# Kernel optimization log

Hardware: AMD Instinct MI355X
Metric: run time of the kernel (lower is better)

## Reference

```python
import jax, jax.numpy as jnp
import numpy as np

DIM = 768
HEADS = 8
HEAD_DIM = DIM // HEADS
SCALE = HEAD_DIM ** -0.5
EPS = 1e-5


def layernorm(x, gamma, beta):
    mu = jnp.mean(x, axis=-1, keepdims=True)
    var = jnp.mean((x - mu) ** 2, axis=-1, keepdims=True)
    return (x - mu) * jax.lax.rsqrt(var + EPS) * gamma + beta


def setup_inputs() -> dict:
    key = jax.random.key(0)
    ks = jax.random.split(key, 12)
    B, L, M, D = 8, 1024, 1024, DIM
    s = D ** -0.5
    return {
        "x": jax.random.normal(ks[0], (B, L, D), jnp.float32),
        "context": jax.random.normal(ks[1], (B, M, D), jnp.float32),
        "Wq": jax.random.normal(ks[2], (D, D), jnp.float32) * s,
        "bq": jnp.zeros((D,), jnp.float32),
        "Wkv": jax.random.normal(ks[3], (D, 2 * D), jnp.float32) * s,
        "bkv": jnp.zeros((2 * D,), jnp.float32),
        "Wp": jax.random.normal(ks[4], (D, D), jnp.float32) * s,
        "bp": jnp.zeros((D,), jnp.float32),
        "g1": jnp.ones((D,), jnp.float32),
        "b1": jnp.zeros((D,), jnp.float32),
        "g2": jnp.ones((D,), jnp.float32),
        "b2": jnp.zeros((D,), jnp.float32),
    }


def reference(x, context, Wq, bq, Wkv, bkv, Wp, bp, g1, b1, g2, b2):
    B, L, D = x.shape
    M = context.shape[1]
    Hp = Wp_ = int(L ** 0.5)
    x_n = layernorm(x, g1, b1)
    c_n = layernorm(context, g2, b2)
    q = (x_n @ Wq + bq).reshape(B, L, HEADS, HEAD_DIM).transpose(0, 2, 1, 3)  # bhld
    kv = (c_n @ Wkv + bkv).reshape(B, M, 2, HEADS, HEAD_DIM).transpose(2, 0, 3, 1, 4)
    k, v = kv[0], kv[1]  # bhmd
    attn = jnp.einsum("bhld,bhmd->bhlm", q, k) * SCALE
    w = jax.nn.softmax(attn, axis=-1)
    attn_map = w.mean(axis=1).sum(axis=-1).reshape(B, Hp, Wp_)
    out = jnp.einsum("bhlm,bhmd->bhld", w, v).transpose(0, 2, 1, 3).reshape(B, L, D)
    out = out @ Wp + bp
    # dropout is identity in eval mode (training=False)
    return out + x, attn_map
```

## Files before the change

kernel.cpp:

```cpp
#include <hip/hip_runtime.h>

typedef unsigned short u16;
typedef short bf16x8 __attribute__((ext_vector_type(8)));
typedef float f32x4 __attribute__((ext_vector_type(4)));
typedef unsigned short u16x8 __attribute__((ext_vector_type(8)));
typedef unsigned short u16x4 __attribute__((ext_vector_type(4)));

union bfr { unsigned int u[4]; bf16x8 v; };

__device__ __forceinline__ u16 f2bf(float f) {
    unsigned int u = __builtin_bit_cast(unsigned int, f);
    u = (u + 0x7fffu + ((u >> 16) & 1u)) >> 16;
    return (u16)u;
}

__device__ __forceinline__ unsigned int cvtpk(float lo, float hi) {
    unsigned int r;
    asm("v_cvt_pk_bf16_f32 %0, %1, %2" : "=v"(r) : "v"(lo), "v"(hi));
    return r;
}

__device__ __forceinline__ void gload16(const u16* src, u16* lds_dst) {
    __builtin_amdgcn_global_load_lds(
        (const __attribute__((address_space(1))) unsigned int*)src,
        (__attribute__((address_space(3))) unsigned int*)lds_dst, 16, 0, 0);
}

__global__ __launch_bounds__(256) void prep_ln_k(
    const float* __restrict__ x, const float* __restrict__ ctx,
    const float* __restrict__ g1, const float* __restrict__ b1,
    const float* __restrict__ g2, const float* __restrict__ b2,
    const float* __restrict__ Wq, const float* __restrict__ Wkv,
    const float* __restrict__ Wp,
    u16* __restrict__ xn, u16* __restrict__ cn,
    u16* __restrict__ WqT, u16* __restrict__ WkvT, u16* __restrict__ WpT)
{
    const int id = blockIdx.x;
    const int t = threadIdx.x;
    if (id >= 16384) {
        __shared__ float T[64][65];
        int t2 = id - 16384;
        const float* src; u16* dst; int lds, k0, n0;
        if (t2 < 288) { src = Wkv; dst = WkvT; lds = 1536; k0 = (t2 / 24) * 64; n0 = (t2 % 24) * 64; }
        else if (t2 < 432) { int u = t2 - 288; src = Wq; dst = WqT; lds = 768; k0 = (u / 12) * 64; n0 = (u % 12) * 64; }
        else { int u = t2 - 432; src = Wp; dst = WpT; lds = 768; k0 = (u / 12) * 64; n0 = (u % 12) * 64; }
        const int rr = t >> 4, c4 = (t & 15) * 4;
        #pragma unroll
        for (int it = 0; it < 4; it++) {
            int r = rr + it * 16;
            f32x4 v = *(const f32x4*)&src[(long)(k0 + r) * lds + n0 + c4];
            #pragma unroll
            for (int j = 0; j < 4; j++) T[c4 + j][r] = v[j];
        }
        __syncthreads();
        #pragma unroll
        for (int it = 0; it < 4; it++) {
            int r = rr + it * 16;
            u16x4 w;
            #pragma unroll
            for (int j = 0; j < 4; j++) w[j] = f2bf(T[r][c4 + j]);
            *(u16x4*)&dst[(long)(n0 + r) * 768 + k0 + c4] = w;
        }
        return;
    }
    const float* src; const float* g; const float* b; u16* dst;
    if (id < 8192) { src = x + (long)id * 768; g = g1; b = b1; dst = xn + (long)id * 768; }
    else { int r = id - 8192; src = ctx + (long)r * 768; g = g2; b = b2; dst = cn + (long)r * 768; }

    int lane = t & 63, wid = t >> 6;
    float v0 = src[t], v1 = src[t + 256], v2 = src[t + 512];
    float s = v0 + v1 + v2;
    for (int o = 32; o; o >>= 1) s += __shfl_xor(s, o);
    __shared__ float r1[4], r2[4];
    if (!lane) r1[wid] = s;
    __syncthreads();
    float mu = (r1[0] + r1[1] + r1[2] + r1[3]) * (1.0f / 768.0f);
    float d0 = v0 - mu, d1 = v1 - mu, d2 = v2 - mu;
    float q = d0 * d0 + d1 * d1 + d2 * d2;
    for (int o = 32; o; o >>= 1) q += __shfl_xor(q, o);
    if (!lane) r2[wid] = q;
    __syncthreads();
    float var = (r2[0] + r2[1] + r2[2] + r2[3]) * (1.0f / 768.0f);
    float rs = rsqrtf(var + 1e-5f);
    dst[t]       = f2bf(d0 * rs * g[t]       + b[t]);
    dst[t + 256] = f2bf(d1 * rs * g[t + 256] + b[t + 256]);
    dst[t + 512] = f2bf(d2 * rs * g[t + 512] + b[t + 512]);
}

__global__ __launch_bounds__(256) void qkv_k(
    const u16* __restrict__ xn, const u16* __restrict__ cn,
    const u16* __restrict__ WqT, const u16* __restrict__ WkvT,
    const float* __restrict__ bq, const float* __restrict__ bkv,
    u16* __restrict__ Qb, u16* __restrict__ Kb, u16* __restrict__ Vt)
{
    __shared__ u16 As[128 * 32];
    __shared__ u16 Bs[128 * 32];
    const int id = blockIdx.x;
    const int swz = (id & 7) * 144 + (id >> 3);
    const int tid = threadIdx.x, lane = tid & 63, wid = tid >> 6;
    const int wr = wid >> 1, wc = wid & 1;
    const int g = lane >> 4, i15 = lane & 15;

    const bool isQ = swz < 384;
    int rt, ct;
    const u16* A; const u16* Bt; const float* bias;
    if (isQ) { rt = swz / 6;  ct = swz % 6;  A = xn; Bt = WqT;  bias = bq; }
    else { int s2 = swz - 384; rt = s2 / 12; ct = s2 % 12; A = cn; Bt = WkvT; bias = bkv; }
    const int row0 = rt * 128, col0 = ct * 128;

    const u16* srcA[2]; const u16* srcB[2]; int ldsOff[2];
    #pragma unroll
    for (int c = 0; c < 2; c++) {
        int P0 = (wid * 2 + c) * 1024;
        int P = P0 + lane * 16;
        int r = P >> 6, colx = (P & 63) >> 1;
        srcA[c] = A  + (long)(row0 + r) * 768 + colx;
        srcB[c] = Bt + (long)(col0 + r) * 768 + colx;
        ldsOff[c] = P0 >> 1;
    }

    f32x4 acc[4][4] = {};
    for (int k0 = 0; k0 < 768; k0 += 32) {
        __syncthreads();
        #pragma unroll
        for (int c = 0; c < 2; c++) {
            gload16(srcA[c] + k0, &As[ldsOff[c]]);
            gload16(srcB[c] + k0, &Bs[ldsOff[c]]);
        }
        __syncthreads();
        bf16x8 av[4], bv[4];
        #pragma unroll
        for (int m = 0; m < 4; m++)
            av[m] = *(const bf16x8*)&As[(wr * 64 + m * 16 + i15) * 32 + g * 8];
        #pragma unroll
        for (int n = 0; n < 4; n++)
            bv[n] = *(const bf16x8*)&Bs[(wc * 64 + n * 16 + i15) * 32 + g * 8];
        #pragma unroll
        for (int m = 0; m < 4; m++)
            #pragma unroll
            for (int n = 0; n < 4; n++)
                acc[m][n] = __builtin_amdgcn_mfma_f32_16x16x32_bf16(av[m], bv[n], acc[m][n], 0, 0, 0);
    }

    float bv4[4];
    #pragma unroll
    for (int n = 0; n < 4; n++) bv4[n] = bias[col0 + wc * 64 + n * 16 + i15];

    #pragma unroll
    for (int m = 0; m < 4; m++) {
        #pragma unroll
        for (int n = 0; n < 4; n++) {
            const int col = col0 + wc * 64 + n * 16 + i15;
            #pragma unroll
            for (int r = 0; r < 4; r++) {
                const int row = row0 + wr * 64 + m * 16 + g * 4 + r;
                float v = acc[m][n][r];
                if (isQ) {
                    v = (v + bv4[n]) * 0.14724444706f;
                    int b = row >> 10, l = row & 1023;
                    int h = col / 96, d = col % 96;
                    Qb[((long)(b * 8 + h) * 1024 + l) * 96 + d] = f2bf(v);
                } else {
                    v += bv4[n];
                    int b = row >> 10, mt = row & 1023;
                    if (col < 768) {
                        int h = col / 96, d = col % 96;
                        Kb[((long)(b * 8 + h) * 1024 + mt) * 96 + d] = f2bf(v);
                    } else {
                        int cc = col - 768;
                        int h = cc / 96, d = cc % 96;
                        Vt[((long)(b * 8 + h) * 96 + d) * 1024 + mt] = f2bf(v);
                    }
                }
            }
        }
    }
}

__global__ __launch_bounds__(256) void flash_k(
    const u16* __restrict__ Qb, const u16* __restrict__ Kb,
    const u16* __restrict__ Vt, u16* __restrict__ Ob)
{
    const int i = blockIdx.x;
    const int s8 = i >> 3;
    const int bh = (i & 7) * 8 + (s8 >> 4);
    const int qt = s8 & 15;
    const int tid = threadIdx.x, lane = tid & 63, wid = tid >> 6;
    const int g = lane >> 4, i15 = lane & 15;

    __shared__ u16 Ks[2][6144];
    __shared__ u16 Vs[2][6144];

    const long baseQK = (long)bh * 98304;
    const u16* Kt  = Kb + baseQK;
    const u16* Vtp = Vt + baseQK;

    bf16x8 qf[3];
    {
        const u16* qrow = Qb + baseQK + (long)(qt * 64 + wid * 16 + i15) * 96 + g * 8;
        qf[0] = *(const bf16x8*)(qrow);
        qf[1] = *(const bf16x8*)(qrow + 32);
        qf[2] = *(const bf16x8*)(qrow + 64);
    }

    int krd[4];
    #pragma unroll
    for (int n = 0; n < 4; n++) {
        int q4 = i15 >> 2, rr = i15 & 3, m = n >> 1;
        int R = (n & 1) ? (m * 32 + ((q4 ^ 2) << 3) + 4 + rr)
                        : (m * 32 + (q4 << 3) + rr);
        krd[n] = R * 32 + g * 8;
    }
    int vrd[6][2];
    #pragma unroll
    for (int n6 = 0; n6 < 6; n6++) {
        int row = n6 * 16 + i15;
        #pragma unroll
        for (int kk = 0; kk < 2; kk++)
            vrd[n6][kk] = row * 64 + ((kk * 32 + g * 8) ^ ((row & 7) << 3));
    }

    int kgo[3], kwr[3], vgo[3], vwr[3];
    #pragma unroll
    for (int it = 0; it < 3; it++) {
        int e = tid + it * 256;
        int r = e / 12, cEl = (e % 12) * 8;
        kgo[it] = r * 96 + cEl;
        kwr[it] = (cEl >> 5) * 2048 + r * 32 + (cEl & 31);
        int d = e >> 3, m8 = (e & 7) * 8;
        vgo[it] = d * 1024 + m8;
        vwr[it] = d * 64 + (m8 ^ ((d & 7) << 3));
    }

    u16x8 kreg[3], vreg[3];
    #pragma unroll
    for (int it = 0; it < 3; it++) {
        kreg[it] = *(const u16x8*)&Kt[kgo[it]];
        vreg[it] = *(const u16x8*)&Vtp[vgo[it]];
    }
    #pragma unroll
    for (int it = 0; it < 3; it++) {
        *(u16x8*)&Ks[0][kwr[it]] = kreg[it];
        *(u16x8*)&Vs[0][vwr[it]] = vreg[it];
    }

    f32x4 o[6] = {};
    float lsum = 0.f;
    int cur = 0;

    for (int t = 0; t < 16; t++) {
        __syncthreads();
        if (t < 15) {
            #pragma unroll
            for (int it = 0; it < 3; it++) {
                kreg[it] = *(const u16x8*)&Kt[(t + 1) * 6144 + kgo[it]];
                vreg[it] = *(const u16x8*)&Vtp[(t + 1) * 64 + vgo[it]];
            }
        }

        f32x4 s[4] = {};
        #pragma unroll
        for (int kd = 0; kd < 3; kd++) {
            #pragma unroll
            for (int n = 0; n < 4; n++) {
                bf16x8 kf = *(const bf16x8*)&Ks[cur][kd * 2048 + krd[n]];
                s[n] = __builtin_amdgcn_mfma_f32_16x16x32_bf16(kf, qf[kd], s[n], 0, 0, 0);
            }
        }

        unsigned int pk[4][2];
        #pragma unroll
        for (int n = 0; n < 4; n++) {
            float p0 = exp2f(s[n][0]), p1 = exp2f(s[n][1]);
            float p2 = exp2f(s[n][2]), p3 = exp2f(s[n][3]);
            lsum += (p0 + p1) + (p2 + p3);
            pk[n][0] = cvtpk(p0, p1);
            pk[n][1] = cvtpk(p2, p3);
        }

        #pragma unroll
        for (int kk = 0; kk < 2; kk++) {
            bfr pa;
            pa.u[0] = pk[kk * 2][0];
            pa.u[1] = pk[kk * 2][1];
            pa.u[2] = __shfl_xor(pk[kk * 2 + 1][0], 32);
            pa.u[3] = __shfl_xor(pk[kk * 2 + 1][1], 32);
            #pragma unroll
            for (int n6 = 0; n6 < 6; n6++) {
                bf16x8 vf = *(const bf16x8*)&Vs[cur][vrd[n6][kk]];
                o[n6] = __builtin_amdgcn_mfma_f32_16x16x32_bf16(pa.v, vf, o[n6], 0, 0, 0);
            }
        }

        if (t < 15) {
            #pragma unroll
            for (int it = 0; it < 3; it++) {
                *(u16x8*)&Ks[cur ^ 1][kwr[it]] = kreg[it];
                *(u16x8*)&Vs[cur ^ 1][vwr[it]] = vreg[it];
            }
        }
        cur ^= 1;
    }

    lsum += __shfl_xor(lsum, 16);
    lsum += __shfl_xor(lsum, 32);
    float linv = 1.0f / lsum;

    const int b = bh >> 3, h = bh & 7;
    #pragma unroll
    for (int r = 0; r < 4; r++) {
        float lr = __shfl(linv, g * 4 + r);
        int row = qt * 64 + wid * 16 + g * 4 + r;
        long base = ((long)(b * 1024 + row)) * 768 + h * 96;
        #pragma unroll
        for (int n6 = 0; n6 < 6; n6++)
            Ob[base + n6 * 16 + i15] = f2bf(o[n6][r] * lr);
    }
}

__global__ __launch_bounds__(256) void out_k(
    const u16* __restrict__ Ob, const u16* __restrict__ WpT,
    const float* __restrict__ bp, const float* __restrict__ resid,
    float* __restrict__ out, float* __restrict__ amap)
{
    const int id = blockIdx.x;
    if (id >= 384) {
        amap[(id - 384) * 256 + threadIdx.x] = 1.0f;
        return;
    }
    const int swz = (id & 7) * 48 + (id >> 3);
    const int rt = swz / 6, ct = swz % 6;
    const int row0 = rt * 128, col0 = ct * 128;
    const int tid = threadIdx.x, lane = tid & 63, wid = tid >> 6;
    const int wr = wid >> 1, wc = wid & 1;
    const int g = lane >> 4, i15 = lane & 15;

    __shared__ u16 As[128 * 32];
    __shared__ u16 Bs[128 * 32];

    const u16* srcA[2]; const u16* srcB[2]; int ldsOff[2];
    #pragma unroll
    for (int c = 0; c < 2; c++) {
        int P0 = (wid * 2 + c) * 1024;
        int P = P0 + lane * 16;
        int r = P >> 6, colx = (P & 63) >> 1;
        srcA[c] = Ob  + (long)(row0 + r) * 768 + colx;
        srcB[c] = WpT + (long)(col0 + r) * 768 + colx;
        ldsOff[c] = P0 >> 1;
    }

    f32x4 acc[4][4] = {};
    for (int k0 = 0; k0 < 768; k0 += 32) {
        __syncthreads();
        #pragma unroll
        for (int c = 0; c < 2; c++) {
            gload16(srcA[c] + k0, &As[ldsOff[c]]);
            gload16(srcB[c] + k0, &Bs[ldsOff[c]]);
        }
        __syncthreads();
        bf16x8 av[4], bv[4];
        #pragma unroll
        for (int m = 0; m < 4; m++)
            av[m] = *(const bf16x8*)&As[(wr * 64 + m * 16 + i15) * 32 + g * 8];
        #pragma unroll
        for (int n = 0; n < 4; n++)
            bv[n] = *(const bf16x8*)&Bs[(wc * 64 + n * 16 + i15) * 32 + g * 8];
        #pragma unroll
        for (int m = 0; m < 4; m++)
            #pragma unroll
            for (int n = 0; n < 4; n++)
                acc[m][n] = __builtin_amdgcn_mfma_f32_16x16x32_bf16(av[m], bv[n], acc[m][n], 0, 0, 0);
    }

    float bv4[4];
    #pragma unroll
    for (int n = 0; n < 4; n++) bv4[n] = bp[col0 + wc * 64 + n * 16 + i15];

    #pragma unroll
    for (int m = 0; m < 4; m++) {
        #pragma unroll
        for (int n = 0; n < 4; n++) {
            const int col = col0 + wc * 64 + n * 16 + i15;
            #pragma unroll
            for (int r = 0; r < 4; r++) {
                const int row = row0 + wr * 64 + m * 16 + g * 4 + r;
                long idx = (long)row * 768 + col;
                out[idx] = acc[m][n][r] + bv4[n] + resid[idx];
            }
        }
    }
}

extern "C" void kernel_launch(void* const* d_in, const int* in_sizes, int n_in,
                              void* d_out, int out_size, void* d_ws, size_t ws_size,
                              hipStream_t stream)
{
    const float* x   = (const float*)d_in[0];
    const float* ctx = (const float*)d_in[1];
    const float* Wq  = (const float*)d_in[2];
    const float* bq  = (const float*)d_in[3];
    const float* Wkv = (const float*)d_in[4];
    const float* bkv = (const float*)d_in[5];
    const float* Wp  = (const float*)d_in[6];
    const float* bp  = (const float*)d_in[7];
    const float* g1  = (const float*)d_in[8];
    const float* b1  = (const float*)d_in[9];
    const float* g2  = (const float*)d_in[10];
    const float* b2  = (const float*)d_in[11];
    float* out = (float*)d_out;

    char* w = (char*)d_ws;
    const long SZ_ROWS = 8192L * 768 * 2;
    long off = 0;
    u16* xn   = (u16*)(w + off); off += SZ_ROWS;
    u16* cn   = (u16*)(w + off); off += SZ_ROWS;
    u16* WqT  = (u16*)(w + off); off += 768L * 768 * 2;
    u16* WkvT = (u16*)(w + off); off += 1536L * 768 * 2;
    u16* WpT  = (u16*)(w + off); off += 768L * 768 * 2;
    u16* Qb   = (u16*)(w + off); off += SZ_ROWS;
    u16* Kb   = (u16*)(w + off); off += SZ_ROWS;
    u16* Vt   = (u16*)(w + off); off += SZ_ROWS;
    u16* Ob   = (u16*)(w + off); off += SZ_ROWS;

    prep_ln_k<<<16960, 256, 0, stream>>>(x, ctx, g1, b1, g2, b2, Wq, Wkv, Wp,
                                         xn, cn, WqT, WkvT, WpT);
    qkv_k<<<1152, 256, 0, stream>>>(xn, cn, WqT, WkvT, bq, bkv, Qb, Kb, Vt);
    flash_k<<<1024, 256, 0, stream>>>(Qb, Kb, Vt, Ob);
    out_k<<<416, 256, 0, stream>>>(Ob, WpT, bp, x, out, out + 6291456L);
}
```

Before: 158.4 us.

## Triple-buffer LDS in projection GEMMs with async prefetch two tiles ahead

```diff
diff --git a/kernel.cpp b/kernel.cpp
--- a/kernel.cpp
+++ b/kernel.cpp
@@ -87,14 +87,47 @@
     dst[t + 512] = f2bf(d2 * rs * g[t + 512] + b[t + 512]);
 }
 
+#define GSTAGE(BUF, T) do {                                          \
+    const int k0_ = (T) * 32;                                        \
+    _Pragma("unroll")                                                \
+    for (int c_ = 0; c_ < 2; c_++) {                                 \
+        gload16(srcA[c_] + k0_, &As[BUF][ldsOff[c_]]);               \
+        gload16(srcB[c_] + k0_, &Bs[BUF][ldsOff[c_]]);               \
+    }                                                                \
+} while (0)
+
+#define GCOMP(BUF) do {                                              \
+    bf16x8 av_[4], bv_[4];                                           \
+    _Pragma("unroll")                                                \
+    for (int m_ = 0; m_ < 4; m_++)                                   \
+        av_[m_] = *(const bf16x8*)&As[BUF][(wr * 64 + m_ * 16 + i15) * 32 + g * 8]; \
+    _Pragma("unroll")                                                \
+    for (int n_ = 0; n_ < 4; n_++)                                   \
+        bv_[n_] = *(const bf16x8*)&Bs[BUF][(wc * 64 + n_ * 16 + i15) * 32 + g * 8]; \
+    _Pragma("unroll")                                                \
+    for (int m_ = 0; m_ < 4; m_++)                                   \
+        _Pragma("unroll")                                            \
+        for (int n_ = 0; n_ < 4; n_++)                               \
+            acc[m_][n_] = __builtin_amdgcn_mfma_f32_16x16x32_bf16(av_[m_], bv_[n_], acc[m_][n_], 0, 0, 0); \
+} while (0)
+
+#define GSTEP(T) do {                                                \
+    if ((T) < 23) asm volatile("s_waitcnt vmcnt(4)" ::: "memory");   \
+    else          asm volatile("s_waitcnt vmcnt(0)" ::: "memory");   \
+    __builtin_amdgcn_s_barrier();                                    \
+    __builtin_amdgcn_sched_barrier(0);                               \
+    if ((T) + 2 < 24) GSTAGE(((T) + 2) % 3, (T) + 2);                \
+    GCOMP((T) % 3);                                                  \
+} while (0)
+
 __global__ __launch_bounds__(256) void qkv_k(
     const u16* __restrict__ xn, const u16* __restrict__ cn,
     const u16* __restrict__ WqT, const u16* __restrict__ WkvT,
     const float* __restrict__ bq, const float* __restrict__ bkv,
     u16* __restrict__ Qb, u16* __restrict__ Kb, u16* __restrict__ Vt)
 {
-    __shared__ u16 As[128 * 32];
-    __shared__ u16 Bs[128 * 32];
+    __shared__ u16 As[3][128 * 32];
+    __shared__ u16 Bs[3][128 * 32];
     const int id = blockIdx.x;
     const int swz = (id & 7) * 144 + (id >> 3);
     const int tid = threadIdx.x, lane = tid & 63, wid = tid >> 6;
@@ -120,27 +153,11 @@
     }
 
     f32x4 acc[4][4] = {};
-    for (int k0 = 0; k0 < 768; k0 += 32) {
-        __syncthreads();
-        #pragma unroll
-        for (int c = 0; c < 2; c++) {
-            gload16(srcA[c] + k0, &As[ldsOff[c]]);
-            gload16(srcB[c] + k0, &Bs[ldsOff[c]]);
-        }
-        __syncthreads();
-        bf16x8 av[4], bv[4];
-        #pragma unroll
-        for (int m = 0; m < 4; m++)
-            av[m] = *(const bf16x8*)&As[(wr * 64 + m * 16 + i15) * 32 + g * 8];
-        #pragma unroll
-        for (int n = 0; n < 4; n++)
-            bv[n] = *(const bf16x8*)&Bs[(wc * 64 + n * 16 + i15) * 32 + g * 8];
-        #pragma unroll
-        for (int m = 0; m < 4; m++)
-            #pragma unroll
-            for (int n = 0; n < 4; n++)
-                acc[m][n] = __builtin_amdgcn_mfma_f32_16x16x32_bf16(av[m], bv[n], acc[m][n], 0, 0, 0);
-    }
+
+    GSTAGE(0, 0);
+    GSTAGE(1, 1);
+    #pragma unroll
+    for (int t = 0; t < 24; t++) GSTEP(t);
 
     float bv4[4];
     #pragma unroll
@@ -328,15 +345,14 @@
         amap[(id - 384) * 256 + threadIdx.x] = 1.0f;
         return;
     }
+    __shared__ u16 As[3][128 * 32];
+    __shared__ u16 Bs[3][128 * 32];
     const int swz = (id & 7) * 48 + (id >> 3);
     const int rt = swz / 6, ct = swz % 6;
     const int row0 = rt * 128, col0 = ct * 128;
     const int tid = threadIdx.x, lane = tid & 63, wid = tid >> 6;
     const int wr = wid >> 1, wc = wid & 1;
     const int g = lane >> 4, i15 = lane & 15;
-
-    __shared__ u16 As[128 * 32];
-    __shared__ u16 Bs[128 * 32];
 
     const u16* srcA[2]; const u16* srcB[2]; int ldsOff[2];
     #pragma unroll
@@ -350,27 +366,11 @@
     }
 
     f32x4 acc[4][4] = {};
-    for (int k0 = 0; k0 < 768; k0 += 32) {
-        __syncthreads();
-        #pragma unroll
-        for (int c = 0; c < 2; c++) {
-            gload16(srcA[c] + k0, &As[ldsOff[c]]);
-            gload16(srcB[c] + k0, &Bs[ldsOff[c]]);
-        }
-        __syncthreads();
-        bf16x8 av[4], bv[4];
-        #pragma unroll
-        for (int m = 0; m < 4; m++)
-            av[m] = *(const bf16x8*)&As[(wr * 64 + m * 16 + i15) * 32 + g * 8];
-        #pragma unroll
-        for (int n = 0; n < 4; n++)
-            bv[n] = *(const bf16x8*)&Bs[(wc * 64 + n * 16 + i15) * 32 + g * 8];
-        #pragma unroll
-        for (int m = 0; m < 4; m++)
-            #pragma unroll
-            for (int n = 0; n < 4; n++)
-                acc[m][n] = __builtin_amdgcn_mfma_f32_16x16x32_bf16(av[m], bv[n], acc[m][n], 0, 0, 0);
-    }
+
+    GSTAGE(0, 0);
+    GSTAGE(1, 1);
+    #pragma unroll
+    for (int t = 0; t < 24; t++) GSTEP(t);
 
     float bv4[4];
     #pragma unroll
```

After: 161.1 us. About the same (+1.7%).

## Restructure QKV GEMM into 256x256 tiles with 4-stage async LDS pipeline

Applied to the files above, without the earlier changes.

```diff
diff --git a/kernel.cpp b/kernel.cpp
--- a/kernel.cpp
+++ b/kernel.cpp
@@ -87,73 +87,98 @@
     dst[t + 512] = f2bf(d2 * rs * g[t + 512] + b[t + 512]);
 }
 
-__global__ __launch_bounds__(256) void qkv_k(
+#define QSTAGE(BUF, T) do {                                           \
+    _Pragma("unroll")                                                 \
+    for (int c_ = 0; c_ < 2; c_++) {                                  \
+        gload16(sA[c_] + (T) * 32, &As[BUF][(wid * 128 + c_ * 64) * 8]); \
+        gload16(sB[c_] + (T) * 32, &Bs[BUF][(wid * 128 + c_ * 64) * 8]); \
+    }                                                                 \
+} while (0)
+
+#define QSTEP(T) do {                                                 \
+    if ((T) < 23) asm volatile("s_waitcnt vmcnt(4)" ::: "memory");    \
+    else          asm volatile("s_waitcnt vmcnt(0)" ::: "memory");    \
+    __builtin_amdgcn_s_barrier();                                     \
+    __builtin_amdgcn_sched_barrier(0);                                \
+    if ((T) + 2 < 24) QSTAGE(((T) + 2) & 3, (T) + 2);                 \
+    bf16x8 av_[8], bv_[4];                                            \
+    _Pragma("unroll")                                                 \
+    for (int m_ = 0; m_ < 8; m_++)                                    \
+        av_[m_] = *(const bf16x8*)&As[(T) & 3][aoff[m_]];             \
+    _Pragma("unroll")                                                 \
+    for (int n_ = 0; n_ < 4; n_++)                                    \
+        bv_[n_] = *(const bf16x8*)&Bs[(T) & 3][boff[n_]];             \
+    __builtin_amdgcn_s_setprio(1);                                    \
+    _Pragma("unroll")                                                 \
+    for (int m_ = 0; m_ < 8; m_++)                                    \
+        _Pragma("unroll")                                             \
+        for (int n_ = 0; n_ < 4; n_++)                                \
+            acc[m_][n_] = __builtin_amdgcn_mfma_f32_16x16x32_bf16(av_[m_], bv_[n_], acc[m_][n_], 0, 0, 0); \
+    __builtin_amdgcn_s_setprio(0);                                    \
+} while (0)
+
+__global__ __launch_bounds__(512, 2) void qkv_k(
     const u16* __restrict__ xn, const u16* __restrict__ cn,
     const u16* __restrict__ WqT, const u16* __restrict__ WkvT,
     const float* __restrict__ bq, const float* __restrict__ bkv,
     u16* __restrict__ Qb, u16* __restrict__ Kb, u16* __restrict__ Vt)
 {
-    __shared__ u16 As[128 * 32];
-    __shared__ u16 Bs[128 * 32];
+    __shared__ u16 As[4][8192];
+    __shared__ u16 Bs[4][8192];
     const int id = blockIdx.x;
-    const int swz = (id & 7) * 144 + (id >> 3);
+    const int swz = (id & 7) * 36 + (id >> 3);
     const int tid = threadIdx.x, lane = tid & 63, wid = tid >> 6;
-    const int wr = wid >> 1, wc = wid & 1;
+    const int wr = wid >> 2, wc = wid & 3;
     const int g = lane >> 4, i15 = lane & 15;
 
-    const bool isQ = swz < 384;
+    const bool isQ = swz < 96;
     int rt, ct;
     const u16* A; const u16* Bt; const float* bias;
-    if (isQ) { rt = swz / 6;  ct = swz % 6;  A = xn; Bt = WqT;  bias = bq; }
-    else { int s2 = swz - 384; rt = s2 / 12; ct = s2 % 12; A = cn; Bt = WkvT; bias = bkv; }
-    const int row0 = rt * 128, col0 = ct * 128;
-
-    const u16* srcA[2]; const u16* srcB[2]; int ldsOff[2];
+    if (isQ) { rt = swz / 3;  ct = swz % 3;  A = xn; Bt = WqT;  bias = bq; }
+    else { int s2 = swz - 96; rt = s2 / 6; ct = s2 % 6; A = cn; Bt = WkvT; bias = bkv; }
+    const int row0 = rt * 256, col0 = ct * 256;
+
+    const u16* sA[2]; const u16* sB[2];
     #pragma unroll
     for (int c = 0; c < 2; c++) {
-        int P0 = (wid * 2 + c) * 1024;
-        int P = P0 + lane * 16;
-        int r = P >> 6, colx = (P & 63) >> 1;
-        srcA[c] = A  + (long)(row0 + r) * 768 + colx;
-        srcB[c] = Bt + (long)(col0 + r) * 768 + colx;
-        ldsOff[c] = P0 >> 1;
-    }
-
-    f32x4 acc[4][4] = {};
-    for (int k0 = 0; k0 < 768; k0 += 32) {
-        __syncthreads();
-        #pragma unroll
-        for (int c = 0; c < 2; c++) {
-            gload16(srcA[c] + k0, &As[ldsOff[c]]);
-            gload16(srcB[c] + k0, &Bs[ldsOff[c]]);
-        }
-        __syncthreads();
-        bf16x8 av[4], bv[4];
-        #pragma unroll
-        for (int m = 0; m < 4; m++)
-            av[m] = *(const bf16x8*)&As[(wr * 64 + m * 16 + i15) * 32 + g * 8];
-        #pragma unroll
-        for (int n = 0; n < 4; n++)
-            bv[n] = *(const bf16x8*)&Bs[(wc * 64 + n * 16 + i15) * 32 + g * 8];
-        #pragma unroll
-        for (int m = 0; m < 4; m++)
-            #pragma unroll
-            for (int n = 0; n < 4; n++)
-                acc[m][n] = __builtin_amdgcn_mfma_f32_16x16x32_bf16(av[m], bv[n], acc[m][n], 0, 0, 0);
-    }
+        int ch = wid * 128 + c * 64 + lane;
+        int r = ch >> 2, sl = ch & 3;
+        int scol = (sl ^ (r & 3)) * 8;
+        sA[c] = A  + (long)(row0 + r) * 768 + scol;
+        sB[c] = Bt + (long)(col0 + r) * 768 + scol;
+    }
+
+    int aoff[8], boff[4];
+    #pragma unroll
+    for (int m = 0; m < 8; m++) {
+        int R = wr * 128 + m * 16 + i15;
+        aoff[m] = R * 32 + (g ^ (R & 3)) * 8;
+    }
+    #pragma unroll
+    for (int n = 0; n < 4; n++) {
+        int R = wc * 64 + n * 16 + i15;
+        boff[n] = R * 32 + (g ^ (R & 3)) * 8;
+    }
+
+    f32x4 acc[8][4] = {};
+
+    QSTAGE(0, 0);
+    QSTAGE(1, 1);
+    #pragma unroll
+    for (int t = 0; t < 24; t++) QSTEP(t);
 
     float bv4[4];
     #pragma unroll
     for (int n = 0; n < 4; n++) bv4[n] = bias[col0 + wc * 64 + n * 16 + i15];
 
     #pragma unroll
-    for (int m = 0; m < 4; m++) {
+    for (int m = 0; m < 8; m++) {
         #pragma unroll
         for (int n = 0; n < 4; n++) {
             const int col = col0 + wc * 64 + n * 16 + i15;
             #pragma unroll
             for (int r = 0; r < 4; r++) {
-                const int row = row0 + wr * 64 + m * 16 + g * 4 + r;
+                const int row = row0 + wr * 128 + m * 16 + g * 4 + r;
                 float v = acc[m][n][r];
                 if (isQ) {
                     v = (v + bv4[n]) * 0.14724444706f;
@@ -328,15 +353,14 @@
         amap[(id - 384) * 256 + threadIdx.x] = 1.0f;
         return;
     }
+    __shared__ u16 As[128 * 32];
+    __shared__ u16 Bs[128 * 32];
     const int swz = (id & 7) * 48 + (id >> 3);
     const int rt = swz / 6, ct = swz % 6;
     const int row0 = rt * 128, col0 = ct * 128;
     const int tid = threadIdx.x, lane = tid & 63, wid = tid >> 6;
     const int wr = wid >> 1, wc = wid & 1;
     const int g = lane >> 4, i15 = lane & 15;
-
-    __shared__ u16 As[128 * 32];
-    __shared__ u16 Bs[128 * 32];
 
     const u16* srcA[2]; const u16* srcB[2]; int ldsOff[2];
     #pragma unroll
@@ -424,7 +448,7 @@
 
     prep_ln_k<<<16960, 256, 0, stream>>>(x, ctx, g1, b1, g2, b2, Wq, Wkv, Wp,
                                          xn, cn, WqT, WkvT, WpT);
-    qkv_k<<<1152, 256, 0, stream>>>(xn, cn, WqT, WkvT, bq, bkv, Qb, Kb, Vt);
+    qkv_k<<<288, 512, 0, stream>>>(xn, cn, WqT, WkvT, bq, bkv, Qb, Kb, Vt);
     flash_k<<<1024, 256, 0, stream>>>(Qb, Kb, Vt, Ob);
     out_k<<<416, 256, 0, stream>>>(Ob, WpT, bp, x, out, out + 6291456L);
 }
```

Measured after the change: 178.2 us. +12.5%, slower.
